# Performance work log

Measured on AMD Instinct MI355X. Metric: run time of the kernel, lower is better.

## Reference

```python
import jax, jax.numpy as jnp
import numpy as np

B, H, D = 4096, 200, 64
HID = 64


def setup_inputs() -> dict:
    key = jax.random.key(0)
    ks = jax.random.split(key, 12)
    s = 1.0 / np.sqrt(HID)
    return {
        "x": jax.random.normal(ks[0], (B, H, D), jnp.float32),
        "pos_query": jax.random.normal(ks[1], (B, D), jnp.float32),
        "lengths": jax.random.randint(ks[2], (B,), 1, H + 1, jnp.int32),
        "W_ih": jax.random.normal(ks[3], (3 * HID, D), jnp.float32) * s,
        "W_hh": jax.random.normal(ks[4], (3 * HID, HID), jnp.float32) * s,
        "b_ih": jax.random.normal(ks[5], (3 * HID,), jnp.float32) * s,
        "b_hh": jax.random.normal(ks[6], (3 * HID,), jnp.float32) * s,
        "aW_ih": jax.random.normal(ks[7], (3 * HID, HID), jnp.float32) * s,
        "aW_hh": jax.random.normal(ks[8], (3 * HID, HID), jnp.float32) * s,
        "ab_ih": jax.random.normal(ks[9], (3 * HID,), jnp.float32) * s,
        "ab_hh": jax.random.normal(ks[10], (3 * HID,), jnp.float32) * s,
    }


def _gates(x_t, h, W_i, W_h, b_i, b_h):
    gi = x_t @ W_i.T + b_i  # (B, 3H), PyTorch gate order [r, z, n]
    gh = h @ W_h.T + b_h
    gir, giz, gin = jnp.split(gi, 3, axis=-1)
    ghr, ghz, ghn = jnp.split(gh, 3, axis=-1)
    r = jax.nn.sigmoid(gir + ghr)
    z = jax.nn.sigmoid(giz + ghz)
    n = jnp.tanh(gin + r * ghn)
    return z, n


def _forward(x, pos_query, lengths, W_ih, W_hh, b_ih, b_hh, aW_ih, aW_hh, ab_ih, ab_hh):
    # mask[t, b] = True for valid (packed) timesteps
    mask = (jnp.arange(H)[:, None] < lengths[None, :])[:, :, None]  # (H, B, 1)
    xt = jnp.swapaxes(x, 0, 1)  # (H, B, D) time-major

    # --- GRU over packed sequence; padded positions output 0 (pad_packed_sequence) ---
    def gru_step(h, inp):
        x_t, m = inp
        z, n = _gates(x_t, h, W_ih, W_hh, b_ih, b_hh)
        h_new = (1.0 - z) * n + z * h
        h = jnp.where(m, h_new, h)
        return h, jnp.where(m, h_new, 0.0)

    h0 = jnp.zeros((x.shape[0], HID), x.dtype)
    _, out = jax.lax.scan(gru_step, h0, (xt, mask))  # out: (H, B, HID)

    # --- attention over full H (padded scores are 0, matching the torch code) ---
    scores = jnp.einsum("bd,hbd->bh", pos_query, out)  # (B, H)
    att = jax.nn.softmax(scores, axis=1)  # (B, H)

    # --- AUGRU: update gate scaled by attention score, masked to valid steps ---
    att_t = att.T[:, :, None]  # (H, B, 1)

    def augru_step(h, inp):
        o_t, a_t, m = inp
        u, n = _gates(o_t, h, aW_ih, aW_hh, ab_ih, ab_hh)
        u = a_t * u
        h_new = (1.0 - u) * h + u * n
        h = jnp.where(m, h_new, h)
        return h, None

    h_last, _ = jax.lax.scan(augru_step, h0, (out, att_t, mask))
    # h frozen past each sequence's length -> h_last == state at t = length-1
    return h_last  # (B, HID)


def reference(x, pos_query, lengths, W_ih, W_hh, b_ih, b_hh, aW_ih, aW_hh, ab_ih, ab_hh):
    return _forward(x, pos_query, lengths, W_ih, W_hh, b_ih, b_hh,
                    aW_ih, aW_hh, ab_ih, ab_hh)
```

## Files before the change

kernel.cpp:

```cpp
#include <hip/hip_runtime.h>
#include <hip/hip_bf16.h>


#define Bq   4096
#define Tq   200
#define BT   8

typedef __attribute__((ext_vector_type(8))) short short8;
typedef __attribute__((ext_vector_type(4))) float f32x4;

#define MFMA(a, b, c) __builtin_amdgcn_mfma_f32_16x16x32_bf16((a), (b), (c), 0, 0, 0)

static __device__ __forceinline__ unsigned pk2(float a, float b) {
  __hip_bfloat162 t = __float22bfloat162_rn(make_float2(a, b));
  unsigned r;
  __builtin_memcpy(&r, &t, sizeof(r));
  return r;
}
static __device__ __forceinline__ void pack4(f32x4 v, uint2 &H, uint2 &L) {
  H.x = pk2(v[0], v[1]);
  H.y = pk2(v[2], v[3]);
  float l0 = v[0] - __uint_as_float(H.x << 16);
  float l1 = v[1] - __uint_as_float(H.x & 0xffff0000u);
  float l2 = v[2] - __uint_as_float(H.y << 16);
  float l3 = v[3] - __uint_as_float(H.y & 0xffff0000u);
  L.x = pk2(l0, l1);
  L.y = pk2(l2, l3);
}
static __device__ __forceinline__ float sigm(float x) {
  return __builtin_amdgcn_rcpf(1.0f + __expf(-x));
}
static __device__ __forceinline__ float tanh_(float x) {
  return 2.0f * __builtin_amdgcn_rcpf(1.0f + __expf(-2.0f * x)) - 1.0f;
}
static __device__ __forceinline__ void split8(f32x4 a, f32x4 b, short8 &hi, short8 &lo) {
  uint2 H, L;
  pack4(a, H, L);
  hi[0] = (short)(H.x & 0xffff); hi[1] = (short)(H.x >> 16);
  hi[2] = (short)(H.y & 0xffff); hi[3] = (short)(H.y >> 16);
  lo[0] = (short)(L.x & 0xffff); lo[1] = (short)(L.x >> 16);
  lo[2] = (short)(L.y & 0xffff); lo[3] = (short)(L.y >> 16);
  pack4(b, H, L);
  hi[4] = (short)(H.x & 0xffff); hi[5] = (short)(H.x >> 16);
  hi[6] = (short)(H.y & 0xffff); hi[7] = (short)(H.y >> 16);
  lo[4] = (short)(L.x & 0xffff); lo[5] = (short)(L.x >> 16);
  lo[6] = (short)(L.y & 0xffff); lo[7] = (short)(L.y >> 16);
}

__global__ __launch_bounds__(256, 2)
void gru_fwd(const float* __restrict__ x, const float* __restrict__ pq,
             const int* __restrict__ lengths,
             const float* __restrict__ Wih, const float* __restrict__ Whh,
             const float* __restrict__ bih, const float* __restrict__ bhh,
             unsigned short* __restrict__ outbf,
             float* __restrict__ scores)
{
  __shared__ alignas(16) unsigned short hbH[2][16][72], hbL[2][16][72];
  __shared__ alignas(16) unsigned short xbH[2][8][72], xbL[2][8][72];
  __shared__ float slds[2][4][8];

  const int tid  = threadIdx.x;
  const int w    = tid >> 6;
  const int lane = tid & 63;
  const int c    = lane & 15;
  const int g    = lane >> 4;
  const int jh   = w * 16;
  const int bl   = c & (BT - 1);
  const int b_g  = blockIdx.x * BT + bl;

  const int pb   = tid >> 5;
  const int pd   = 2 * (tid & 31);
  const int pb_g = blockIdx.x * BT + pb;

  for (int i = tid; i < 16 * 72; i += 256) {
    hbH[0][0][i] = 0; hbL[0][0][i] = 0;
  }
  {
    float2 f = *(const float2*)(x + (size_t)pb_g * Tq * 64 + pd);
    unsigned H = pk2(f.x, f.y);
    float l0 = f.x - __uint_as_float(H << 16);
    float l1 = f.y - __uint_as_float(H & 0xffff0000u);
    *(unsigned*)&xbH[0][pb][pd] = H;
    *(unsigned*)&xbL[0][pb][pd] = pk2(l0, l1);
  }

  short8 wiH[3][2], wiL[3][2], whH[3][2], whL[3][2];
#pragma unroll
  for (int gt = 0; gt < 3; ++gt)
#pragma unroll
    for (int kc = 0; kc < 2; ++kc) {
      const float* p = Wih + (size_t)(gt * 64 + jh + c) * 64 + kc * 32 + g * 8;
      split8(*(const f32x4*)p, *(const f32x4*)(p + 4), wiH[gt][kc], wiL[gt][kc]);
      const float* q = Whh + (size_t)(gt * 64 + jh + c) * 64 + kc * 32 + g * 8;
      split8(*(const f32x4*)q, *(const f32x4*)(q + 4), whH[gt][kc], whL[gt][kc]);
    }

  f32x4 bR, bZ, bNi, bNh;
  {
    f32x4 bi0 = *(const f32x4*)(bih + 0 * 64 + jh + 4 * g);
    f32x4 bh0 = *(const f32x4*)(bhh + 0 * 64 + jh + 4 * g);
    f32x4 bi1 = *(const f32x4*)(bih + 1 * 64 + jh + 4 * g);
    f32x4 bh1 = *(const f32x4*)(bhh + 1 * 64 + jh + 4 * g);
    bR = bi0 + bh0; bZ = bi1 + bh1;
    bNi = *(const f32x4*)(bih + 2 * 64 + jh + 4 * g);
    bNh = *(const f32x4*)(bhh + 2 * 64 + jh + 4 * g);
  }
  const f32x4 pqv = *(const f32x4*)(pq + (size_t)b_g * 64 + jh + 4 * g);
  const int len = lengths[b_g];

  f32x4 hreg = {0.f, 0.f, 0.f, 0.f};
  __syncthreads();

  for (int t = 0; t < Tq; ++t) {
    const int cur = t & 1, nxt = cur ^ 1;

    float2 xf = make_float2(0.f, 0.f);
    if (t + 1 < Tq)
      xf = *(const float2*)(x + (size_t)pb_g * Tq * 64 + (size_t)(t + 1) * 64 + pd);

    short8 xH[2], xL[2], hH[2], hL[2];
#pragma unroll
    for (int kc = 0; kc < 2; ++kc) {
      xH[kc] = *(const short8*)&xbH[cur][bl][kc * 32 + g * 8];
      xL[kc] = *(const short8*)&xbL[cur][bl][kc * 32 + g * 8];
      hH[kc] = *(const short8*)&hbH[cur][c][kc * 32 + g * 8];
      hL[kc] = *(const short8*)&hbL[cur][c][kc * 32 + g * 8];
    }

    if (t > 0 && w == 0 && lane < BT) {
      float s = slds[nxt][0][lane] + slds[nxt][1][lane] +
                slds[nxt][2][lane] + slds[nxt][3][lane];
      scores[(size_t)(blockIdx.x * BT + lane) * Tq + (t - 1)] = s;
    }

    f32x4 aR = bR, aZ = bZ, aNi = bNi, aNh = bNh;
#pragma unroll
    for (int kc = 0; kc < 2; ++kc) {
      aR = MFMA(wiH[0][kc], xH[kc], aR);
      aR = MFMA(wiH[0][kc], xL[kc], aR);
      aR = MFMA(wiL[0][kc], xH[kc], aR);
      aR = MFMA(whH[0][kc], hH[kc], aR);
      aR = MFMA(whH[0][kc], hL[kc], aR);
      aR = MFMA(whL[0][kc], hH[kc], aR);
      aZ = MFMA(wiH[1][kc], xH[kc], aZ);
      aZ = MFMA(wiH[1][kc], xL[kc], aZ);
      aZ = MFMA(wiL[1][kc], xH[kc], aZ);
      aZ = MFMA(whH[1][kc], hH[kc], aZ);
      aZ = MFMA(whH[1][kc], hL[kc], aZ);
      aZ = MFMA(whL[1][kc], hH[kc], aZ);
      aNi = MFMA(wiH[2][kc], xH[kc], aNi);
      aNi = MFMA(wiH[2][kc], xL[kc], aNi);
      aNi = MFMA(wiL[2][kc], xH[kc], aNi);
      aNh = MFMA(whH[2][kc], hH[kc], aNh);
      aNh = MFMA(whH[2][kc], hL[kc], aNh);
      aNh = MFMA(whL[2][kc], hH[kc], aNh);
    }

    const bool valid = t < len;
    f32x4 outv;
#pragma unroll
    for (int r = 0; r < 4; ++r) {
      float rr = sigm(aR[r]);
      float zz = sigm(aZ[r]);
      float nn = tanh_(aNi[r] + rr * aNh[r]);
      float hn = (1.f - zz) * nn + zz * hreg[r];
      hreg[r] = valid ? hn : hreg[r];
      outv[r] = valid ? hn : 0.f;
    }

    {
      uint2 H, L;
      pack4(hreg, H, L);
      *(uint2*)&hbH[nxt][c][jh + 4 * g] = H;
      *(uint2*)&hbL[nxt][c][jh + 4 * g] = L;
    }

    float sp = outv[0] * pqv[0] + outv[1] * pqv[1] + outv[2] * pqv[2] + outv[3] * pqv[3];
    sp += __shfl_xor(sp, 16);
    sp += __shfl_xor(sp, 32);
    if (lane < BT) slds[cur][w][lane] = sp;

    if (c < BT) {
      uint2 O;
      O.x = pk2(outv[0], outv[1]);
      O.y = pk2(outv[2], outv[3]);
      *(uint2*)(outbf + (size_t)t * Bq * 64 + (size_t)b_g * 64 + jh + 4 * g) = O;
    }

    {
      unsigned H = pk2(xf.x, xf.y);
      float l0 = xf.x - __uint_as_float(H << 16);
      float l1 = xf.y - __uint_as_float(H & 0xffff0000u);
      *(unsigned*)&xbH[nxt][pb][pd] = H;
      *(unsigned*)&xbL[nxt][pb][pd] = pk2(l0, l1);
    }

    __syncthreads();
  }

  if (w == 0 && lane < BT) {
    const int pb2 = (Tq - 1) & 1;
    float s = slds[pb2][0][lane] + slds[pb2][1][lane] +
              slds[pb2][2][lane] + slds[pb2][3][lane];
    scores[(size_t)(blockIdx.x * BT + lane) * Tq + (Tq - 1)] = s;
  }
}

__global__ __launch_bounds__(256)
void softmax_att(const float* __restrict__ scores, float* __restrict__ att)
{
  const int w = threadIdx.x >> 6, lane = threadIdx.x & 63;
  const int row = blockIdx.x * 4 + w;
  const float* s = scores + (size_t)row * Tq;
  float v0 = s[lane], v1 = s[lane + 64], v2 = s[lane + 128];
  float v3 = (lane < Tq - 192) ? s[lane + 192] : -1e30f;
  float m = fmaxf(fmaxf(v0, v1), fmaxf(v2, v3));
#pragma unroll
  for (int off = 32; off >= 1; off >>= 1) m = fmaxf(m, __shfl_xor(m, off));
  float e0 = __expf(v0 - m), e1 = __expf(v1 - m), e2 = __expf(v2 - m);
  float e3 = (lane < Tq - 192) ? __expf(v3 - m) : 0.f;
  float sum = e0 + e1 + e2 + e3;
#pragma unroll
  for (int off = 32; off >= 1; off >>= 1) sum += __shfl_xor(sum, off);
  float inv = 1.f / sum;
  float* a = att + (size_t)row * Tq;
  a[lane] = e0 * inv;
  a[lane + 64] = e1 * inv;
  a[lane + 128] = e2 * inv;
  if (lane < Tq - 192) a[lane + 192] = e3 * inv;
}

__global__ __launch_bounds__(256, 2)
void augru_fwd(const unsigned short* __restrict__ outbf, const float* __restrict__ att,
               const int* __restrict__ lengths,
               const float* __restrict__ Wih, const float* __restrict__ Whh,
               const float* __restrict__ bih, const float* __restrict__ bhh,
               float* __restrict__ hout)
{
  __shared__ alignas(16) unsigned short hbH[2][16][72], hbL[2][16][72];
  __shared__ float att_lds[BT][204];

  const int tid  = threadIdx.x;
  const int w    = tid >> 6;
  const int lane = tid & 63;
  const int c    = lane & 15;
  const int g    = lane >> 4;
  const int jh   = w * 16;
  const int bl   = c & (BT - 1);
  const int b_g  = blockIdx.x * BT + bl;

  for (int i = tid; i < 16 * 72; i += 256) {
    hbH[0][0][i] = 0; hbL[0][0][i] = 0;
  }
  for (int i = tid; i < BT * Tq; i += 256)
    att_lds[i / Tq][i % Tq] = att[(size_t)blockIdx.x * BT * Tq + i];

  short8 wiH[3][2], wiL[3][2], whH[3][2], whL[3][2];
#pragma unroll
  for (int gt = 0; gt < 3; ++gt)
#pragma unroll
    for (int kc = 0; kc < 2; ++kc) {
      const float* p = Wih + (size_t)(gt * 64 + jh + c) * 64 + kc * 32 + g * 8;
      split8(*(const f32x4*)p, *(const f32x4*)(p + 4), wiH[gt][kc], wiL[gt][kc]);
      const float* q = Whh + (size_t)(gt * 64 + jh + c) * 64 + kc * 32 + g * 8;
      split8(*(const f32x4*)q, *(const f32x4*)(q + 4), whH[gt][kc], whL[gt][kc]);
    }

  f32x4 bR, bZ, bNi, bNh;
  {
    f32x4 bi0 = *(const f32x4*)(bih + 0 * 64 + jh + 4 * g);
    f32x4 bh0 = *(const f32x4*)(bhh + 0 * 64 + jh + 4 * g);
    f32x4 bi1 = *(const f32x4*)(bih + 1 * 64 + jh + 4 * g);
    f32x4 bh1 = *(const f32x4*)(bhh + 1 * 64 + jh + 4 * g);
    bR = bi0 + bh0; bZ = bi1 + bh1;
    bNi = *(const f32x4*)(bih + 2 * 64 + jh + 4 * g);
    bNh = *(const f32x4*)(bhh + 2 * 64 + jh + 4 * g);
  }
  const int len = lengths[b_g];

  short8 xcur[2];
#pragma unroll
  for (int kc = 0; kc < 2; ++kc)
    xcur[kc] = *(const short8*)(outbf + (size_t)b_g * 64 + kc * 32 + g * 8);

  f32x4 hreg = {0.f, 0.f, 0.f, 0.f};
  __syncthreads();

  for (int t = 0; t < Tq; ++t) {
    const int cur = t & 1, nxt = cur ^ 1;

    short8 xnxt[2];
    if (t + 1 < Tq) {
#pragma unroll
      for (int kc = 0; kc < 2; ++kc)
        xnxt[kc] = *(const short8*)(outbf + (size_t)(t + 1) * Bq * 64 +
                                    (size_t)b_g * 64 + kc * 32 + g * 8);
    } else {
      xnxt[0] = xcur[0]; xnxt[1] = xcur[1];
    }

    short8 hH[2], hL[2];
#pragma unroll
    for (int kc = 0; kc < 2; ++kc) {
      hH[kc] = *(const short8*)&hbH[cur][c][kc * 32 + g * 8];
      hL[kc] = *(const short8*)&hbL[cur][c][kc * 32 + g * 8];
    }
    const float a_t = att_lds[bl][t];

    f32x4 aR = bR, aZ = bZ, aNi = bNi, aNh = bNh;
#pragma unroll
    for (int kc = 0; kc < 2; ++kc) {
      aR = MFMA(wiH[0][kc], xcur[kc], aR);
      aR = MFMA(wiL[0][kc], xcur[kc], aR);
      aR = MFMA(whH[0][kc], hH[kc], aR);
      aR = MFMA(whH[0][kc], hL[kc], aR);
      aR = MFMA(whL[0][kc], hH[kc], aR);
      aZ = MFMA(wiH[1][kc], xcur[kc], aZ);
      aZ = MFMA(wiL[1][kc], xcur[kc], aZ);
      aZ = MFMA(whH[1][kc], hH[kc], aZ);
      aZ = MFMA(whH[1][kc], hL[kc], aZ);
      aZ = MFMA(whL[1][kc], hH[kc], aZ);
      aNi = MFMA(wiH[2][kc], xcur[kc], aNi);
      aNi = MFMA(wiL[2][kc], xcur[kc], aNi);
      aNh = MFMA(whH[2][kc], hH[kc], aNh);
      aNh = MFMA(whH[2][kc], hL[kc], aNh);
      aNh = MFMA(whL[2][kc], hH[kc], aNh);
    }

    const bool valid = t < len;
#pragma unroll
    for (int r = 0; r < 4; ++r) {
      float rr = sigm(aR[r]);
      float uu = a_t * sigm(aZ[r]);
      float nn = tanh_(aNi[r] + rr * aNh[r]);
      float hn = (1.f - uu) * hreg[r] + uu * nn;
      hreg[r] = valid ? hn : hreg[r];
    }

    {
      uint2 H, L;
      pack4(hreg, H, L);
      *(uint2*)&hbH[nxt][c][jh + 4 * g] = H;
      *(uint2*)&hbL[nxt][c][jh + 4 * g] = L;
    }

    xcur[0] = xnxt[0]; xcur[1] = xnxt[1];
    __syncthreads();
  }

  if (c < BT)
    *(f32x4*)(hout + (size_t)b_g * 64 + jh + 4 * g) = hreg;
}

extern "C" void kernel_launch(void* const* d_in, const int* in_sizes, int n_in,
                              void* d_out, int out_size, void* d_ws, size_t ws_size,
                              hipStream_t stream)
{
  const float* x       = (const float*)d_in[0];
  const float* pq      = (const float*)d_in[1];
  const int*   lengths = (const int*)d_in[2];
  const float* Wih     = (const float*)d_in[3];
  const float* Whh     = (const float*)d_in[4];
  const float* bih     = (const float*)d_in[5];
  const float* bhh     = (const float*)d_in[6];
  const float* aWih    = (const float*)d_in[7];
  const float* aWhh    = (const float*)d_in[8];
  const float* abih    = (const float*)d_in[9];
  const float* abhh    = (const float*)d_in[10];
  float* hout = (float*)d_out;

  char* ws = (char*)d_ws;
  unsigned short* outbf = (unsigned short*)ws;
  float* scores = (float*)(ws + (size_t)Tq * Bq * 64 * 2);
  float* att    = scores + (size_t)Bq * Tq;

  gru_fwd<<<Bq / BT, 256, 0, stream>>>(x, pq, lengths, Wih, Whh, bih, bhh, outbf, scores);
  softmax_att<<<Bq / 4, 256, 0, stream>>>(scores, att);
  augru_fwd<<<Bq / BT, 256, 0, stream>>>(outbf, att, lengths, aWih, aWhh, abih, abhh, hout);
}
```

Baseline: 695.8 us.

## Fill full MFMA tile with 16 batches and pipeline input-gate MFMAs off critical path

Raises the batch tile from 8 to 16 so every MFMA column holds a real sequence, which halves the grid, and drops the wasted half-tile work. Input-projection MFMAs for step t+1 are now computed after the current step's gate math, so only the hidden-state MFMAs sit on the serial dependency chain. The x prefetch is moved two steps ahead, LDS buffers are XOR-swizzled to avoid bank conflicts, and the plain __syncthreads is replaced by an lgkmcnt wait plus s_barrier. Occupancy hint drops to 1 block/SM. With half as many blocks, fewer waves are available to hide latency, and register pressure rises.

Result: faster. 598.2 us (-14.0%).

```diff
diff --git a/kernel.cpp b/kernel.cpp
--- a/kernel.cpp
+++ b/kernel.cpp
@@ -4,12 +4,25 @@
 
 #define Bq   4096
 #define Tq   200
-#define BT   8
+#define BT   16
 
 typedef __attribute__((ext_vector_type(8))) short short8;
 typedef __attribute__((ext_vector_type(4))) float f32x4;
 
 #define MFMA(a, b, c) __builtin_amdgcn_mfma_f32_16x16x32_bf16((a), (b), (c), 0, 0, 0)
+
+#define LGKM_BARRIER()                                      \
+  do {                                                      \
+    __builtin_amdgcn_sched_barrier(0);                      \
+    asm volatile("s_waitcnt lgkmcnt(0)" ::: "memory");      \
+    __builtin_amdgcn_s_barrier();                           \
+    asm volatile("" ::: "memory");                          \
+    __builtin_amdgcn_sched_barrier(0);                      \
+  } while (0)
+
+static __device__ __forceinline__ int swz(int row, int colshort) {
+  return row * 64 + ((((colshort) << 1) ^ ((row & 7) << 4)) >> 1);
+}
 
 static __device__ __forceinline__ unsigned pk2(float a, float b) {
   __hip_bfloat162 t = __float22bfloat162_rn(make_float2(a, b));
@@ -47,7 +60,68 @@
   lo[6] = (short)(L.y & 0xffff); lo[7] = (short)(L.y >> 16);
 }
 
-__global__ __launch_bounds__(256, 2)
+#define GI_X18(dR, dZ, dN, XH, XL)                   \
+  _Pragma("unroll")                                  \
+  for (int kc = 0; kc < 2; ++kc) {                   \
+    dR = MFMA(wiH[0][kc], XH[kc], dR);               \
+    dR = MFMA(wiH[0][kc], XL[kc], dR);               \
+    dR = MFMA(wiL[0][kc], XH[kc], dR);               \
+    dZ = MFMA(wiH[1][kc], XH[kc], dZ);               \
+    dZ = MFMA(wiH[1][kc], XL[kc], dZ);               \
+    dZ = MFMA(wiL[1][kc], XH[kc], dZ);               \
+    dN = MFMA(wiH[2][kc], XH[kc], dN);               \
+    dN = MFMA(wiH[2][kc], XL[kc], dN);               \
+    dN = MFMA(wiL[2][kc], XH[kc], dN);               \
+  }
+
+#define GI_X12(dR, dZ, dN, XB)                       \
+  _Pragma("unroll")                                  \
+  for (int kc = 0; kc < 2; ++kc) {                   \
+    dR = MFMA(wiH[0][kc], XB[kc], dR);               \
+    dR = MFMA(wiL[0][kc], XB[kc], dR);               \
+    dZ = MFMA(wiH[1][kc], XB[kc], dZ);               \
+    dZ = MFMA(wiL[1][kc], XB[kc], dZ);               \
+    dN = MFMA(wiH[2][kc], XB[kc], dN);               \
+    dN = MFMA(wiL[2][kc], XB[kc], dN);               \
+  }
+
+#define GH18(dR, dZ, dNh)                            \
+  _Pragma("unroll")                                  \
+  for (int kc = 0; kc < 2; ++kc) {                   \
+    dR  = MFMA(whH[0][kc], hH[kc], dR);              \
+    dR  = MFMA(whH[0][kc], hL[kc], dR);              \
+    dR  = MFMA(whL[0][kc], hH[kc], dR);              \
+    dZ  = MFMA(whH[1][kc], hH[kc], dZ);              \
+    dZ  = MFMA(whH[1][kc], hL[kc], dZ);              \
+    dZ  = MFMA(whL[1][kc], hH[kc], dZ);              \
+    dNh = MFMA(whH[2][kc], hH[kc], dNh);             \
+    dNh = MFMA(whH[2][kc], hL[kc], dNh);             \
+    dNh = MFMA(whL[2][kc], hH[kc], dNh);             \
+  }
+
+#define LOAD_WEIGHTS(WI, WH)                                                  \
+  _Pragma("unroll")                                                           \
+  for (int gt = 0; gt < 3; ++gt)                                              \
+  _Pragma("unroll")                                                           \
+    for (int kc = 0; kc < 2; ++kc) {                                          \
+      const float* p = WI + (size_t)(gt * 64 + jh + c) * 64 + kc * 32 + g * 8;\
+      split8(*(const f32x4*)p, *(const f32x4*)(p + 4), wiH[gt][kc], wiL[gt][kc]); \
+      const float* q = WH + (size_t)(gt * 64 + jh + c) * 64 + kc * 32 + g * 8;\
+      split8(*(const f32x4*)q, *(const f32x4*)(q + 4), whH[gt][kc], whL[gt][kc]); \
+    }
+
+#define LOAD_BIASES(BI, BH)                                                   \
+  {                                                                           \
+    f32x4 bi0 = *(const f32x4*)(BI + 0 * 64 + jh + 4 * g);                    \
+    f32x4 bh0 = *(const f32x4*)(BH + 0 * 64 + jh + 4 * g);                    \
+    f32x4 bi1 = *(const f32x4*)(BI + 1 * 64 + jh + 4 * g);                    \
+    f32x4 bh1 = *(const f32x4*)(BH + 1 * 64 + jh + 4 * g);                    \
+    bR = bi0 + bh0; bZ = bi1 + bh1;                                           \
+    bNi = *(const f32x4*)(BI + 2 * 64 + jh + 4 * g);                          \
+    bNh = *(const f32x4*)(BH + 2 * 64 + jh + 4 * g);                          \
+  }
+
+__global__ __launch_bounds__(256, 1)
 void gru_fwd(const float* __restrict__ x, const float* __restrict__ pq,
              const int* __restrict__ lengths,
              const float* __restrict__ Wih, const float* __restrict__ Whh,
@@ -55,9 +129,9 @@
              unsigned short* __restrict__ outbf,
              float* __restrict__ scores)
 {
-  __shared__ alignas(16) unsigned short hbH[2][16][72], hbL[2][16][72];
-  __shared__ alignas(16) unsigned short xbH[2][8][72], xbL[2][8][72];
-  __shared__ float slds[2][4][8];
+  __shared__ alignas(16) unsigned short hbH[2][1024], hbL[2][1024];
+  __shared__ alignas(16) unsigned short xbH[2][1024], xbL[2][1024];
+  __shared__ float slds[2][4][16];
 
   const int tid  = threadIdx.x;
   const int w    = tid >> 6;
@@ -65,104 +139,86 @@
   const int c    = lane & 15;
   const int g    = lane >> 4;
   const int jh   = w * 16;
-  const int bl   = c & (BT - 1);
-  const int b_g  = blockIdx.x * BT + bl;
-
-  const int pb   = tid >> 5;
-  const int pd   = 2 * (tid & 31);
+  const int b_g  = blockIdx.x * BT + c;
+
+  const int pb   = tid >> 4;
+  const int pd   = 4 * (tid & 15);
   const int pb_g = blockIdx.x * BT + pb;
 
-  for (int i = tid; i < 16 * 72; i += 256) {
-    hbH[0][0][i] = 0; hbL[0][0][i] = 0;
-  }
-  {
-    float2 f = *(const float2*)(x + (size_t)pb_g * Tq * 64 + pd);
-    unsigned H = pk2(f.x, f.y);
-    float l0 = f.x - __uint_as_float(H << 16);
-    float l1 = f.y - __uint_as_float(H & 0xffff0000u);
-    *(unsigned*)&xbH[0][pb][pd] = H;
-    *(unsigned*)&xbL[0][pb][pd] = pk2(l0, l1);
+  for (int i = tid; i < 1024; i += 256) { hbH[0][i] = 0; hbL[0][i] = 0; }
+
+#pragma unroll
+  for (int t0 = 0; t0 < 2; ++t0) {
+    f32x4 xf = *(const f32x4*)(x + (size_t)pb_g * Tq * 64 + t0 * 64 + pd);
+    uint2 H, L; pack4(xf, H, L);
+    const int si = swz(pb, pd);
+    *(uint2*)&xbH[t0][si] = H;
+    *(uint2*)&xbL[t0][si] = L;
   }
 
   short8 wiH[3][2], wiL[3][2], whH[3][2], whL[3][2];
-#pragma unroll
-  for (int gt = 0; gt < 3; ++gt)
-#pragma unroll
-    for (int kc = 0; kc < 2; ++kc) {
-      const float* p = Wih + (size_t)(gt * 64 + jh + c) * 64 + kc * 32 + g * 8;
-      split8(*(const f32x4*)p, *(const f32x4*)(p + 4), wiH[gt][kc], wiL[gt][kc]);
-      const float* q = Whh + (size_t)(gt * 64 + jh + c) * 64 + kc * 32 + g * 8;
-      split8(*(const f32x4*)q, *(const f32x4*)(q + 4), whH[gt][kc], whL[gt][kc]);
-    }
-
+  LOAD_WEIGHTS(Wih, Whh);
   f32x4 bR, bZ, bNi, bNh;
-  {
-    f32x4 bi0 = *(const f32x4*)(bih + 0 * 64 + jh + 4 * g);
-    f32x4 bh0 = *(const f32x4*)(bhh + 0 * 64 + jh + 4 * g);
-    f32x4 bi1 = *(const f32x4*)(bih + 1 * 64 + jh + 4 * g);
-    f32x4 bh1 = *(const f32x4*)(bhh + 1 * 64 + jh + 4 * g);
-    bR = bi0 + bh0; bZ = bi1 + bh1;
-    bNi = *(const f32x4*)(bih + 2 * 64 + jh + 4 * g);
-    bNh = *(const f32x4*)(bhh + 2 * 64 + jh + 4 * g);
-  }
+  LOAD_BIASES(bih, bhh);
   const f32x4 pqv = *(const f32x4*)(pq + (size_t)b_g * 64 + jh + 4 * g);
   const int len = lengths[b_g];
 
+  __syncthreads();
+
+  f32x4 giR = bR, giZ = bZ, giN = bNi;
+  {
+    short8 xH[2], xL[2];
+#pragma unroll
+    for (int kc = 0; kc < 2; ++kc) {
+      const int si = swz(c, kc * 32 + g * 8);
+      xH[kc] = *(const short8*)&xbH[0][si];
+      xL[kc] = *(const short8*)&xbL[0][si];
+    }
+    GI_X18(giR, giZ, giN, xH, xL);
+  }
+
   f32x4 hreg = {0.f, 0.f, 0.f, 0.f};
-  __syncthreads();
 
   for (int t = 0; t < Tq; ++t) {
     const int cur = t & 1, nxt = cur ^ 1;
-
-    float2 xf = make_float2(0.f, 0.f);
-    if (t + 1 < Tq)
-      xf = *(const float2*)(x + (size_t)pb_g * Tq * 64 + (size_t)(t + 1) * 64 + pd);
-
-    short8 xH[2], xL[2], hH[2], hL[2];
+    const bool more = (t + 1 < Tq);
+
+    f32x4 xf = {0.f, 0.f, 0.f, 0.f};
+    if (t + 2 < Tq)
+      xf = *(const f32x4*)(x + (size_t)pb_g * Tq * 64 + (size_t)(t + 2) * 64 + pd);
+
+    short8 hH[2], hL[2], xnH[2], xnL[2];
 #pragma unroll
     for (int kc = 0; kc < 2; ++kc) {
-      xH[kc] = *(const short8*)&xbH[cur][bl][kc * 32 + g * 8];
-      xL[kc] = *(const short8*)&xbL[cur][bl][kc * 32 + g * 8];
-      hH[kc] = *(const short8*)&hbH[cur][c][kc * 32 + g * 8];
-      hL[kc] = *(const short8*)&hbL[cur][c][kc * 32 + g * 8];
-    }
-
-    if (t > 0 && w == 0 && lane < BT) {
+      const int si = swz(c, kc * 32 + g * 8);
+      hH[kc] = *(const short8*)&hbH[cur][si];
+      hL[kc] = *(const short8*)&hbL[cur][si];
+    }
+    if (more) {
+#pragma unroll
+      for (int kc = 0; kc < 2; ++kc) {
+        const int si = swz(c, kc * 32 + g * 8);
+        xnH[kc] = *(const short8*)&xbH[nxt][si];
+        xnL[kc] = *(const short8*)&xbL[nxt][si];
+      }
+    }
+
+    if (t > 0 && w == 0 && lane < 16) {
       float s = slds[nxt][0][lane] + slds[nxt][1][lane] +
                 slds[nxt][2][lane] + slds[nxt][3][lane];
       scores[(size_t)(blockIdx.x * BT + lane) * Tq + (t - 1)] = s;
     }
 
-    f32x4 aR = bR, aZ = bZ, aNi = bNi, aNh = bNh;
-#pragma unroll
-    for (int kc = 0; kc < 2; ++kc) {
-      aR = MFMA(wiH[0][kc], xH[kc], aR);
-      aR = MFMA(wiH[0][kc], xL[kc], aR);
-      aR = MFMA(wiL[0][kc], xH[kc], aR);
-      aR = MFMA(whH[0][kc], hH[kc], aR);
-      aR = MFMA(whH[0][kc], hL[kc], aR);
-      aR = MFMA(whL[0][kc], hH[kc], aR);
-      aZ = MFMA(wiH[1][kc], xH[kc], aZ);
-      aZ = MFMA(wiH[1][kc], xL[kc], aZ);
-      aZ = MFMA(wiL[1][kc], xH[kc], aZ);
-      aZ = MFMA(whH[1][kc], hH[kc], aZ);
-      aZ = MFMA(whH[1][kc], hL[kc], aZ);
-      aZ = MFMA(whL[1][kc], hH[kc], aZ);
-      aNi = MFMA(wiH[2][kc], xH[kc], aNi);
-      aNi = MFMA(wiH[2][kc], xL[kc], aNi);
-      aNi = MFMA(wiL[2][kc], xH[kc], aNi);
-      aNh = MFMA(whH[2][kc], hH[kc], aNh);
-      aNh = MFMA(whH[2][kc], hL[kc], aNh);
-      aNh = MFMA(whL[2][kc], hH[kc], aNh);
-    }
+    f32x4 aNh = bNh;
+    GH18(giR, giZ, aNh);
 
     const bool valid = t < len;
     f32x4 outv;
 #pragma unroll
     for (int r = 0; r < 4; ++r) {
-      float rr = sigm(aR[r]);
-      float zz = sigm(aZ[r]);
-      float nn = tanh_(aNi[r] + rr * aNh[r]);
+      float rr = sigm(giR[r]);
+      float zz = sigm(giZ[r]);
+      float nn = tanh_(giN[r] + rr * aNh[r]);
       float hn = (1.f - zz) * nn + zz * hreg[r];
       hreg[r] = valid ? hn : hreg[r];
       outv[r] = valid ? hn : 0.f;
@@ -171,34 +227,38 @@
     {
       uint2 H, L;
       pack4(hreg, H, L);
-      *(uint2*)&hbH[nxt][c][jh + 4 * g] = H;
-      *(uint2*)&hbL[nxt][c][jh + 4 * g] = L;
+      const int si = swz(c, jh + 4 * g);
+      *(uint2*)&hbH[nxt][si] = H;
+      *(uint2*)&hbL[nxt][si] = L;
     }
 
     float sp = outv[0] * pqv[0] + outv[1] * pqv[1] + outv[2] * pqv[2] + outv[3] * pqv[3];
     sp += __shfl_xor(sp, 16);
     sp += __shfl_xor(sp, 32);
-    if (lane < BT) slds[cur][w][lane] = sp;
-
-    if (c < BT) {
+    if (lane < 16) slds[cur][w][lane] = sp;
+
+    {
       uint2 O;
       O.x = pk2(outv[0], outv[1]);
       O.y = pk2(outv[2], outv[3]);
       *(uint2*)(outbf + (size_t)t * Bq * 64 + (size_t)b_g * 64 + jh + 4 * g) = O;
     }
 
-    {
-      unsigned H = pk2(xf.x, xf.y);
-      float l0 = xf.x - __uint_as_float(H << 16);
-      float l1 = xf.y - __uint_as_float(H & 0xffff0000u);
-      *(unsigned*)&xbH[nxt][pb][pd] = H;
-      *(unsigned*)&xbL[nxt][pb][pd] = pk2(l0, l1);
-    }
-
-    __syncthreads();
-  }
-
-  if (w == 0 && lane < BT) {
+    f32x4 nR = bR, nZ = bZ, nN = bNi;
+    if (more) { GI_X18(nR, nZ, nN, xnH, xnL); }
+
+    if (t + 2 < Tq) {
+      uint2 H, L; pack4(xf, H, L);
+      const int si = swz(pb, pd);
+      *(uint2*)&xbH[cur][si] = H;
+      *(uint2*)&xbL[cur][si] = L;
+    }
+
+    LGKM_BARRIER();
+    giR = nR; giZ = nZ; giN = nN;
+  }
+
+  if (w == 0 && lane < 16) {
     const int pb2 = (Tq - 1) & 1;
     float s = slds[pb2][0][lane] + slds[pb2][1][lane] +
               slds[pb2][2][lane] + slds[pb2][3][lane];
@@ -230,15 +290,15 @@
   if (lane < Tq - 192) a[lane + 192] = e3 * inv;
 }
 
-__global__ __launch_bounds__(256, 2)
+__global__ __launch_bounds__(256, 1)
 void augru_fwd(const unsigned short* __restrict__ outbf, const float* __restrict__ att,
                const int* __restrict__ lengths,
                const float* __restrict__ Wih, const float* __restrict__ Whh,
                const float* __restrict__ bih, const float* __restrict__ bhh,
                float* __restrict__ hout)
 {
-  __shared__ alignas(16) unsigned short hbH[2][16][72], hbL[2][16][72];
-  __shared__ float att_lds[BT][204];
+  __shared__ alignas(16) unsigned short hbH[2][1024], hbL[2][1024];
+  __shared__ float att_lds[16][201];
 
   const int tid  = threadIdx.x;
   const int w    = tid >> 6;
@@ -246,93 +306,60 @@
   const int c    = lane & 15;
   const int g    = lane >> 4;
   const int jh   = w * 16;
-  const int bl   = c & (BT - 1);
-  const int b_g  = blockIdx.x * BT + bl;
-
-  for (int i = tid; i < 16 * 72; i += 256) {
-    hbH[0][0][i] = 0; hbL[0][0][i] = 0;
-  }
+  const int b_g  = blockIdx.x * BT + c;
+
+  for (int i = tid; i < 1024; i += 256) { hbH[0][i] = 0; hbL[0][i] = 0; }
   for (int i = tid; i < BT * Tq; i += 256)
     att_lds[i / Tq][i % Tq] = att[(size_t)blockIdx.x * BT * Tq + i];
 
   short8 wiH[3][2], wiL[3][2], whH[3][2], whL[3][2];
-#pragma unroll
-  for (int gt = 0; gt < 3; ++gt)
-#pragma unroll
-    for (int kc = 0; kc < 2; ++kc) {
-      const float* p = Wih + (size_t)(gt * 64 + jh + c) * 64 + kc * 32 + g * 8;
-      split8(*(const f32x4*)p, *(const f32x4*)(p + 4), wiH[gt][kc], wiL[gt][kc]);
-      const float* q = Whh + (size_t)(gt * 64 + jh + c) * 64 + kc * 32 + g * 8;
-      split8(*(const f32x4*)q, *(const f32x4*)(q + 4), whH[gt][kc], whL[gt][kc]);
-    }
-
+  LOAD_WEIGHTS(Wih, Whh);
   f32x4 bR, bZ, bNi, bNh;
+  LOAD_BIASES(bih, bhh);
+  const int len = lengths[b_g];
+
+  f32x4 giR = bR, giZ = bZ, giN = bNi;
   {
-    f32x4 bi0 = *(const f32x4*)(bih + 0 * 64 + jh + 4 * g);
-    f32x4 bh0 = *(const f32x4*)(bhh + 0 * 64 + jh + 4 * g);
-    f32x4 bi1 = *(const f32x4*)(bih + 1 * 64 + jh + 4 * g);
-    f32x4 bh1 = *(const f32x4*)(bhh + 1 * 64 + jh + 4 * g);
-    bR = bi0 + bh0; bZ = bi1 + bh1;
-    bNi = *(const f32x4*)(bih + 2 * 64 + jh + 4 * g);
-    bNh = *(const f32x4*)(bhh + 2 * 64 + jh + 4 * g);
-  }
-  const int len = lengths[b_g];
-
-  short8 xcur[2];
-#pragma unroll
-  for (int kc = 0; kc < 2; ++kc)
-    xcur[kc] = *(const short8*)(outbf + (size_t)b_g * 64 + kc * 32 + g * 8);
+    short8 x0[2];
+#pragma unroll
+    for (int kc = 0; kc < 2; ++kc)
+      x0[kc] = *(const short8*)(outbf + (size_t)b_g * 64 + kc * 32 + g * 8);
+    GI_X12(giR, giZ, giN, x0);
+  }
 
   f32x4 hreg = {0.f, 0.f, 0.f, 0.f};
   __syncthreads();
 
   for (int t = 0; t < Tq; ++t) {
     const int cur = t & 1, nxt = cur ^ 1;
-
-    short8 xnxt[2];
-    if (t + 1 < Tq) {
+    const bool more = (t + 1 < Tq);
+
+    short8 xn[2];
+    if (more) {
 #pragma unroll
       for (int kc = 0; kc < 2; ++kc)
-        xnxt[kc] = *(const short8*)(outbf + (size_t)(t + 1) * Bq * 64 +
-                                    (size_t)b_g * 64 + kc * 32 + g * 8);
-    } else {
-      xnxt[0] = xcur[0]; xnxt[1] = xcur[1];
+        xn[kc] = *(const short8*)(outbf + (size_t)(t + 1) * Bq * 64 +
+                                  (size_t)b_g * 64 + kc * 32 + g * 8);
     }
 
     short8 hH[2], hL[2];
 #pragma unroll
     for (int kc = 0; kc < 2; ++kc) {
-      hH[kc] = *(const short8*)&hbH[cur][c][kc * 32 + g * 8];
-      hL[kc] = *(const short8*)&hbL[cur][c][kc * 32 + g * 8];
-    }
-    const float a_t = att_lds[bl][t];
-
-    f32x4 aR = bR, aZ = bZ, aNi = bNi, aNh = bNh;
-#pragma unroll
-    for (int kc = 0; kc < 2; ++kc) {
-      aR = MFMA(wiH[0][kc], xcur[kc], aR);
-      aR = MFMA(wiL[0][kc], xcur[kc], aR);
-      aR = MFMA(whH[0][kc], hH[kc], aR);
-      aR = MFMA(whH[0][kc], hL[kc], aR);
-      aR = MFMA(whL[0][kc], hH[kc], aR);
-      aZ = MFMA(wiH[1][kc], xcur[kc], aZ);
-      aZ = MFMA(wiL[1][kc], xcur[kc], aZ);
-      aZ = MFMA(whH[1][kc], hH[kc], aZ);
-      aZ = MFMA(whH[1][kc], hL[kc], aZ);
-      aZ = MFMA(whL[1][kc], hH[kc], aZ);
-      aNi = MFMA(wiH[2][kc], xcur[kc], aNi);
-      aNi = MFMA(wiL[2][kc], xcur[kc], aNi);
-      aNh = MFMA(whH[2][kc], hH[kc], aNh);
-      aNh = MFMA(whH[2][kc], hL[kc], aNh);
-      aNh = MFMA(whL[2][kc], hH[kc], aNh);
-    }
+      const int si = swz(c, kc * 32 + g * 8);
+      hH[kc] = *(const short8*)&hbH[cur][si];
+      hL[kc] = *(const short8*)&hbL[cur][si];
+    }
+    const float a_t = att_lds[c][t];
+
+    f32x4 aNh = bNh;
+    GH18(giR, giZ, aNh);
 
     const bool valid = t < len;
 #pragma unroll
     for (int r = 0; r < 4; ++r) {
-      float rr = sigm(aR[r]);
-      float uu = a_t * sigm(aZ[r]);
-      float nn = tanh_(aNi[r] + rr * aNh[r]);
+      float rr = sigm(giR[r]);
+      float uu = a_t * sigm(giZ[r]);
+      float nn = tanh_(giN[r] + rr * aNh[r]);
       float hn = (1.f - uu) * hreg[r] + uu * nn;
       hreg[r] = valid ? hn : hreg[r];
     }
@@ -340,16 +367,19 @@
     {
       uint2 H, L;
       pack4(hreg, H, L);
-      *(uint2*)&hbH[nxt][c][jh + 4 * g] = H;
-      *(uint2*)&hbL[nxt][c][jh + 4 * g] = L;
-    }
-
-    xcur[0] = xnxt[0]; xcur[1] = xnxt[1];
-    __syncthreads();
-  }
-
-  if (c < BT)
-    *(f32x4*)(hout + (size_t)b_g * 64 + jh + 4 * g) = hreg;
+      const int si = swz(c, jh + 4 * g);
+      *(uint2*)&hbH[nxt][si] = H;
+      *(uint2*)&hbL[nxt][si] = L;
+    }
+
+    f32x4 nR = bR, nZ = bZ, nN = bNi;
+    if (more) { GI_X12(nR, nZ, nN, xn); }
+
+    LGKM_BARRIER();
+    giR = nR; giZ = nZ; giN = nN;
+  }
+
+  *(f32x4*)(hout + (size_t)b_g * 64 + jh + 4 * g) = hreg;
 }
 
 extern "C" void kernel_launch(void* const* d_in, const int* in_sizes, int n_in,
```
